# Kernel tuning notes

Hardware: AMD Instinct MI355X
Metric: run time of the kernel (lower is better)

Reference implementation:

```python
import jax, jax.numpy as jnp
import numpy as np
from jax import lax

OUT_SCALE = 0.001


def setup_inputs() -> dict:
    key = jax.random.key(0)
    kz, kx = jax.random.split(key)
    z = jax.random.normal(kz, (64, 256, 7, 7), dtype=jnp.float32)
    x = jax.random.normal(kx, (64, 256, 31, 31), dtype=jnp.float32)
    return {"z": z, "x": x}


def reference(z, x):
    # depthwise cross-correlation: each (batch, channel) slice of z is slid
    # over the matching slice of x. Implemented as a grouped conv with
    # feature_group_count = B*C, exactly mirroring torch F.conv2d(groups=B*C).
    B, C, kh, kw = z.shape
    H, W = x.shape[2], x.shape[3]
    x_r = x.reshape(1, B * C, H, W)           # [1, B*C, H, W]
    k_r = z.reshape(B * C, 1, kh, kw)          # [B*C, 1, kh, kw] (OIHW)
    out = lax.conv_general_dilated(
        x_r, k_r,
        window_strides=(1, 1),
        padding="VALID",
        feature_group_count=B * C,
        dimension_numbers=("NCHW", "OIHW", "NCHW"),
    )  # [1, B*C, H-kh+1, W-kw+1]
    out = out.reshape(B, C, out.shape[2], out.shape[3])
    return out * OUT_SCALE
```

## Files before the change

### kernel.cpp

```cpp
#include <hip/hip_runtime.h>


#define KH 7
#define KW 7
#define XH 31
#define XW 31
#define OH 25
#define OW 25
#define NSLICE (64 * 256)

__global__ __launch_bounds__(128)
void xcorr_dw_kernel(const float* __restrict__ z,
                     const float* __restrict__ x,
                     float* __restrict__ out) {
    const int s   = blockIdx.x;
    const int tid = threadIdx.x;

    __shared__ float xs[XH * XW];
    __shared__ float zs[KH * KW];

    const float* __restrict__ xg = x + (size_t)s * (XH * XW);
    const float* __restrict__ zg = z + (size_t)s * (KH * KW);

    for (int idx = tid; idx < XH * XW; idx += 128) xs[idx] = xg[idx];
    if (tid < KH * KW) zs[tid] = zg[tid];
    __syncthreads();

    if (tid < 125) {
        float zr[KH * KW];
        #pragma unroll
        for (int k = 0; k < KH * KW; ++k) zr[k] = zs[k];

        const int oy  = tid / 5;
        const int ox0 = (tid % 5) * 5;

        float acc[5] = {0.f, 0.f, 0.f, 0.f, 0.f};
        #pragma unroll
        for (int i = 0; i < KH; ++i) {
            const int rowbase = (oy + i) * XW + ox0;
            float r[KW + 4];
            #pragma unroll
            for (int j = 0; j < KW + 4; ++j) r[j] = xs[rowbase + j];
            #pragma unroll
            for (int j = 0; j < KW; ++j) {
                const float w = zr[i * KW + j];
                #pragma unroll
                for (int k = 0; k < 5; ++k)
                    acc[k] = fmaf(r[j + k], w, acc[k]);
            }
        }

        float* __restrict__ og = out + (size_t)s * (OH * OW) + tid * 5;
        #pragma unroll
        for (int k = 0; k < 5; ++k) og[k] = acc[k] * 0.001f;
    }
}

extern "C" void kernel_launch(void* const* d_in, const int* in_sizes, int n_in,
                              void* d_out, int out_size, void* d_ws, size_t ws_size,
                              hipStream_t stream) {
    const float* z = (const float*)d_in[0];
    const float* x = (const float*)d_in[1];
    float* out = (float*)d_out;
    xcorr_dw_kernel<<<dim3(NSLICE), dim3(128), 0, stream>>>(z, x, out);
}
```

Baseline: 131.1 us.

## Pack five slices per block with 5x5 register output tiles

Each block now handles five slices instead of one, and each thread computes a 5x5 output tile instead of a 1x5 strip. Each input row loaded into registers is reused across up to five output rows, which cuts shared-memory reads per FMA. Shared memory rows are padded to a stride of 35 to reduce bank conflicts. In exchange each thread holds more registers (25 accumulators and 49 weights), and the global staging loop pays for integer division, while the grid becomes about five times smaller.

```diff
diff --git a/kernel.cpp b/kernel.cpp
--- a/kernel.cpp
+++ b/kernel.cpp
@@ -8,51 +8,76 @@
 #define OH 25
 #define OW 25
 #define NSLICE (64 * 256)
+#define SPB 5
+#define THREADS 128
+#define XSTRIDE 35
+#define XSLICE (XH * XSTRIDE)
 
-__global__ __launch_bounds__(128)
+__global__ __launch_bounds__(THREADS)
 void xcorr_dw_kernel(const float* __restrict__ z,
                      const float* __restrict__ x,
                      float* __restrict__ out) {
-    const int s   = blockIdx.x;
     const int tid = threadIdx.x;
+    const int base_slice = blockIdx.x * SPB;
+    const int nsl = min(SPB, NSLICE - base_slice);
 
-    __shared__ float xs[XH * XW];
-    __shared__ float zs[KH * KW];
+    __shared__ float xs[SPB * XSLICE];
+    __shared__ float zs[SPB * KH * KW];
 
-    const float* __restrict__ xg = x + (size_t)s * (XH * XW);
-    const float* __restrict__ zg = z + (size_t)s * (KH * KW);
-
-    for (int idx = tid; idx < XH * XW; idx += 128) xs[idx] = xg[idx];
-    if (tid < KH * KW) zs[tid] = zg[tid];
+    const float* __restrict__ xg = x + (size_t)base_slice * (XH * XW);
+    const float* __restrict__ zg = z + (size_t)base_slice * (KH * KW);
+    const int nx = nsl * (XH * XW);
+    for (int idx = tid; idx < nx; idx += THREADS) {
+        const int sl  = idx / (XH * XW);
+        const int rem = idx - sl * (XH * XW);
+        const int row = rem / XW;
+        const int col = rem - row * XW;
+        xs[sl * XSLICE + row * XSTRIDE + col] = xg[idx];
+    }
+    const int nz = nsl * (KH * KW);
+    for (int idx = tid; idx < nz; idx += THREADS) zs[idx] = zg[idx];
     __syncthreads();
 
-    if (tid < 125) {
+    const int sl = tid / 25;
+    const int tt = tid - sl * 25;
+    if (sl < nsl) {
         float zr[KH * KW];
         #pragma unroll
-        for (int k = 0; k < KH * KW; ++k) zr[k] = zs[k];
+        for (int k = 0; k < KH * KW; ++k) zr[k] = zs[sl * (KH * KW) + k];
 
-        const int oy  = tid / 5;
-        const int ox0 = (tid % 5) * 5;
+        const int oy0 = (tt / 5) * 5;
+        const int ox0 = (tt % 5) * 5;
+        const float* __restrict__ xsp = &xs[sl * XSLICE + oy0 * XSTRIDE + ox0];
 
-        float acc[5] = {0.f, 0.f, 0.f, 0.f, 0.f};
+        float acc[5][5] = {};
         #pragma unroll
-        for (int i = 0; i < KH; ++i) {
-            const int rowbase = (oy + i) * XW + ox0;
-            float r[KW + 4];
+        for (int r = 0; r < 11; ++r) {
+            float xr[11];
             #pragma unroll
-            for (int j = 0; j < KW + 4; ++j) r[j] = xs[rowbase + j];
+            for (int c = 0; c < 11; ++c) xr[c] = xsp[r * XSTRIDE + c];
             #pragma unroll
-            for (int j = 0; j < KW; ++j) {
-                const float w = zr[i * KW + j];
-                #pragma unroll
-                for (int k = 0; k < 5; ++k)
-                    acc[k] = fmaf(r[j + k], w, acc[k]);
+            for (int a = 0; a < 5; ++a) {
+                const int i = r - a;
+                if (i >= 0 && i < KH) {
+                    #pragma unroll
+                    for (int j = 0; j < KW; ++j) {
+                        const float w = zr[i * KW + j];
+                        #pragma unroll
+                        for (int b = 0; b < 5; ++b)
+                            acc[a][b] = fmaf(xr[j + b], w, acc[a][b]);
+                    }
+                }
             }
         }
 
-        float* __restrict__ og = out + (size_t)s * (OH * OW) + tid * 5;
+        float* __restrict__ og =
+            out + (size_t)(base_slice + sl) * (OH * OW) + oy0 * OW + ox0;
         #pragma unroll
-        for (int k = 0; k < 5; ++k) og[k] = acc[k] * 0.001f;
+        for (int a = 0; a < 5; ++a) {
+            #pragma unroll
+            for (int b = 0; b < 5; ++b)
+                og[a * OW + b] = acc[a][b] * 0.001f;
+        }
     }
 }
 
@@ -62,5 +87,6 @@
     const float* z = (const float*)d_in[0];
     const float* x = (const float*)d_in[1];
     float* out = (float*)d_out;
-    xcorr_dw_kernel<<<dim3(NSLICE), dim3(128), 0, stream>>>(z, x, out);
+    const int nblk = (NSLICE + SPB - 1) / SPB;
+    xcorr_dw_kernel<<<dim3(nblk), dim3(THREADS), 0, stream>>>(z, x, out);
 }
```

Result: faster. 126.3 us (-3.6%).

## Map one thread per output column, streaming input rows from global memory

Applied to the files above, without the earlier changes.

Replaces the per-slice shared-memory tiling with one thread per output column. Each thread keeps all 49 filter weights in registers, reads 7-wide input row windows directly from global memory with vector loads, and accumulates 25 output rows in registers as a sliding column. This drops the LDS staging, the block barrier and the idle threads of the 128-thread blocks, and fills the launch with full 256-thread blocks. In exchange it relies on the cache to absorb overlapping row reads between neighbouring threads, uses float4 loads that are not 16-byte aligned, and needs more registers per thread.

```diff
diff --git a/kernel.cpp b/kernel.cpp
--- a/kernel.cpp
+++ b/kernel.cpp
@@ -8,52 +8,49 @@
 #define OH 25
 #define OW 25
 #define NSLICE (64 * 256)
+#define THREADS 256
 
-__global__ __launch_bounds__(128)
+__global__ __launch_bounds__(THREADS)
 void xcorr_dw_kernel(const float* __restrict__ z,
                      const float* __restrict__ x,
                      float* __restrict__ out) {
-    const int s   = blockIdx.x;
-    const int tid = threadIdx.x;
+    const int t = blockIdx.x * THREADS + threadIdx.x;
+    const int s  = t / OW;
+    const int ox = t - s * OW;
 
-    __shared__ float xs[XH * XW];
-    __shared__ float zs[KH * KW];
+    const float* __restrict__ zgp = z + (size_t)s * (KH * KW);
+    float zr[KH * KW];
+    #pragma unroll
+    for (int k = 0; k < 12; ++k) {
+        const float4 v = *(const float4*)(zgp + 4 * k);
+        zr[4 * k + 0] = v.x; zr[4 * k + 1] = v.y;
+        zr[4 * k + 2] = v.z; zr[4 * k + 3] = v.w;
+    }
+    zr[48] = zgp[48];
 
-    const float* __restrict__ xg = x + (size_t)s * (XH * XW);
-    const float* __restrict__ zg = z + (size_t)s * (KH * KW);
+    const float* __restrict__ xgp = x + (size_t)s * (XH * XW) + ox;
+    float acc[OH] = {};
+    #pragma unroll
+    for (int r = 0; r < XH; ++r) {
+        const float* __restrict__ p = xgp + r * XW;
+        const float4 a = *(const float4*)(p);
+        const float4 b = *(const float4*)(p + 3);
+        const float f[KW] = {a.x, a.y, a.z, a.w, b.y, b.z, b.w};
+        const int lo = (r - (KH - 1) < 0) ? 0 : r - (KH - 1);
+        const int hi = (r < OH - 1) ? r : OH - 1;
+        #pragma unroll
+        for (int oy = lo; oy <= hi; ++oy) {
+            const int i = r - oy;
+            #pragma unroll
+            for (int j = 0; j < KW; ++j)
+                acc[oy] = fmaf(f[j], zr[i * KW + j], acc[oy]);
+        }
+    }
 
-    for (int idx = tid; idx < XH * XW; idx += 128) xs[idx] = xg[idx];
-    if (tid < KH * KW) zs[tid] = zg[tid];
-    __syncthreads();
-
-    if (tid < 125) {
-        float zr[KH * KW];
-        #pragma unroll
-        for (int k = 0; k < KH * KW; ++k) zr[k] = zs[k];
-
-        const int oy  = tid / 5;
-        const int ox0 = (tid % 5) * 5;
-
-        float acc[5] = {0.f, 0.f, 0.f, 0.f, 0.f};
-        #pragma unroll
-        for (int i = 0; i < KH; ++i) {
-            const int rowbase = (oy + i) * XW + ox0;
-            float r[KW + 4];
-            #pragma unroll
-            for (int j = 0; j < KW + 4; ++j) r[j] = xs[rowbase + j];
-            #pragma unroll
-            for (int j = 0; j < KW; ++j) {
-                const float w = zr[i * KW + j];
-                #pragma unroll
-                for (int k = 0; k < 5; ++k)
-                    acc[k] = fmaf(r[j + k], w, acc[k]);
-            }
-        }
-
-        float* __restrict__ og = out + (size_t)s * (OH * OW) + tid * 5;
-        #pragma unroll
-        for (int k = 0; k < 5; ++k) og[k] = acc[k] * 0.001f;
-    }
+    float* __restrict__ og = out + (size_t)s * (OH * OW) + ox;
+    #pragma unroll
+    for (int oy = 0; oy < OH; ++oy)
+        og[oy * OW] = acc[oy] * 0.001f;
 }
 
 extern "C" void kernel_launch(void* const* d_in, const int* in_sizes, int n_in,
@@ -62,5 +59,7 @@
     const float* z = (const float*)d_in[0];
     const float* x = (const float*)d_in[1];
     float* out = (float*)d_out;
-    xcorr_dw_kernel<<<dim3(NSLICE), dim3(128), 0, stream>>>(z, x, out);
+    const int nthreads = NSLICE * OW;
+    const int nblk = nthreads / THREADS;
+    xcorr_dw_kernel<<<dim3(nblk), dim3(THREADS), 0, stream>>>(z, x, out);
 }
```

New measurement: 125.3 us. 1.05x faster.
